# Kernel optimization log

Measured on AMD Instinct MI355X. Metric: run time of the kernel, lower is better.

Reference implementation:

```python
import jax, jax.numpy as jnp
import numpy as np

BN_EPS = 1e-5

def _ste_sign(x):
    # forward: sign in {-1,+1}; backward: clipped straight-through (grad 1 on [-1,1])
    s = jnp.where(x >= 0, 1.0, -1.0).astype(x.dtype)
    c = jnp.clip(x, -1.0, 1.0)
    return c + jax.lax.stop_gradient(s - c)

def setup_inputs() -> dict:
    key = jax.random.key(0)
    ks = jax.random.split(key, 8)
    N, C, H, W = 32, 256, 56, 56
    x = jax.random.normal(ks[0], (N, C, H, W), dtype=jnp.float32)
    bias0 = jax.random.normal(ks[1], (C,), dtype=jnp.float32) * 0.1
    w = jax.random.normal(ks[2], (C, C, 1, 1), dtype=jnp.float32) * 0.05
    gamma = jnp.ones((C,), dtype=jnp.float32)
    beta = jnp.zeros((C,), dtype=jnp.float32)
    bias1 = jax.random.normal(ks[3], (C,), dtype=jnp.float32) * 0.1
    alpha = jnp.full((C,), 0.25, dtype=jnp.float32)  # PReLU init
    bias2 = jax.random.normal(ks[4], (C,), dtype=jnp.float32) * 0.1
    return {"x": x, "bias0": bias0, "w": w, "gamma": gamma, "beta": beta,
            "bias1": bias1, "alpha": alpha, "bias2": bias2}

def reference(x, bias0, w, gamma, beta, bias1, alpha, bias2):
    ch = lambda v: v[None, :, None, None]
    # move0: learnable per-channel bias
    out = x + ch(bias0)
    # binary activation: sign (STE)
    out = _ste_sign(out)
    # binarized 1x1 conv: w_bin = mean(|w|) per out-channel * sign(w)
    scale = jnp.mean(jnp.abs(w), axis=(1, 2, 3))              # [O]
    wb = scale[:, None] * _ste_sign(w[:, :, 0, 0])            # [O, C]
    out = jnp.einsum('nchw,oc->nohw', out, wb)                # 1x1 conv
    # bn1: batch statistics (training-mode math)
    mu = jnp.mean(out, axis=(0, 2, 3), keepdims=True)
    var = jnp.var(out, axis=(0, 2, 3), keepdims=True)
    out = ch(gamma) * (out - mu) * jax.lax.rsqrt(var + BN_EPS) + ch(beta)
    # residual add (downsample is None)
    out = out + x
    # move1 -> PReLU -> move2
    out = out + ch(bias1)
    out = jnp.where(out > 0, out, ch(alpha) * out)
    out = out + ch(bias2)
    return out
```

## Files before the change

kernel.cpp:

```cpp
#include <hip/hip_runtime.h>
#include <stdint.h>

typedef unsigned long long u64;
typedef unsigned int u32;

constexpr int kC  = 256;
constexpr int kHW = 3136;
constexpr int kN  = 32;
constexpr int kP  = kN * kHW;
constexpr int kPB = 64;
constexpr int kBlocks = kP / kPB;

constexpr size_t OFF_T     = 0;
constexpr size_t OFF_SCALE = 8192;
constexpr size_t OFF_SUMD  = 9216;
constexpr size_t OFF_SUMD2 = 11264;
constexpr size_t OFF_S     = 13312;

__global__ __launch_bounds__(256) void prep_kernel(
    const float* __restrict__ w, char* __restrict__ ws) {
  u64*   T     = (u64*)(ws + OFF_T);
  float* scale = (float*)(ws + OFF_SCALE);
  u64*   sumd  = (u64*)(ws + OFF_SUMD);
  u64*   sumd2 = (u64*)(ws + OFF_SUMD2);

  int o = threadIdx.x;
  const float* wr = w + o * kC;
  float acc = 0.0f;
  u64 bits[4] = {0, 0, 0, 0};
#pragma unroll 8
  for (int c = 0; c < kC; ++c) {
    float v = wr[c];
    acc += fabsf(v);
    if (v >= 0.0f) bits[c >> 6] |= (1ull << (c & 63));
  }
  scale[o] = acc * (1.0f / 256.0f);
#pragma unroll
  for (int k = 0; k < 4; ++k) T[k * 256 + o] = bits[k];
  sumd[o]  = 0ull;
  sumd2[o] = 0ull;
}

__global__ __launch_bounds__(256) void pack_stats_kernel(
    const float* __restrict__ x, const float* __restrict__ bias0,
    char* __restrict__ ws) {
  __shared__ u64 ldsS[4][kPB];

  int t     = threadIdx.x;
  int pos   = t & 63;
  int chunk = t >> 6;

  u32 p  = blockIdx.x * (u32)kPB + (u32)pos;
  u32 n  = p / kHW;
  u32 hw = p - n * kHW;
  const float* xp = x + (size_t)n * kC * kHW + (size_t)(chunk * 64) * kHW + hw;
  const float* bp = bias0 + chunk * 64;

  u64 bits = 0;
#pragma unroll 16
  for (int i = 0; i < 64; ++i) {
    float v = xp[(size_t)i * kHW] + bp[i];
    if (v >= 0.0f) bits |= (1ull << i);
  }

  u64* S = (u64*)(ws + OFF_S);
  S[(size_t)chunk * kP + p] = bits;
  ldsS[chunk][pos] = bits;
  __syncthreads();

  const u64* T = (const u64*)(ws + OFF_T);
  u64 t0 = T[t], t1 = T[256 + t], t2 = T[512 + t], t3 = T[768 + t];
  int summ = 0, summ2 = 0;
#pragma unroll 8
  for (int pp = 0; pp < kPB; ++pp) {
    int k = __popcll(ldsS[0][pp] ^ t0) + __popcll(ldsS[1][pp] ^ t1) +
            __popcll(ldsS[2][pp] ^ t2) + __popcll(ldsS[3][pp] ^ t3);
    int m = 128 - k;
    summ  += m;
    summ2 += m * m;
  }
  u64* sumd  = (u64*)(ws + OFF_SUMD);
  u64* sumd2 = (u64*)(ws + OFF_SUMD2);
  atomicAdd(&sumd[t],  (u64)(long long)(2 * summ));
  atomicAdd(&sumd2[t], (u64)(long long)(4 * summ2));
}

__global__ __launch_bounds__(256) void finalize_kernel(
    const float* __restrict__ x, const float* __restrict__ gamma,
    const float* __restrict__ beta, const float* __restrict__ bias1,
    const float* __restrict__ alpha, const float* __restrict__ bias2,
    const char* __restrict__ ws, float* __restrict__ out) {
  __shared__ u64    ldsT[4][256];
  __shared__ float4 ldsC[256];

  int t = threadIdx.x;
  {
    const u64* T = (const u64*)(ws + OFF_T);
#pragma unroll
    for (int k = 0; k < 4; ++k) ldsT[k][t] = T[k * 256 + t];

    const float*     scale = (const float*)(ws + OFF_SCALE);
    const long long* sumd  = (const long long*)(ws + OFF_SUMD);
    const long long* sumd2 = (const long long*)(ws + OFF_SUMD2);
    double inv  = 1.0 / (double)kP;
    double md   = (double)sumd[t] * inv;
    double e2   = (double)sumd2[t] * inv;
    double vard = e2 - md * md;
    float sc  = scale[t];
    float mu  = sc * (float)md;
    float var = sc * sc * (float)vard;
    float rs  = rsqrtf(var + 1e-5f);
    float g   = gamma[t];
    float cA  = g * rs * sc;
    float cB  = beta[t] - g * rs * mu + bias1[t];
    ldsC[t] = make_float4(2.0f * cA, cB, alpha[t], bias2[t]);
  }
  __syncthreads();

  int pos   = t & 63;
  int chunk = t >> 6;
  u32 p  = blockIdx.x * (u32)kPB + (u32)pos;
  u32 n  = p / kHW;
  u32 hw = p - n * kHW;

  const u64* S = (const u64*)(ws + OFF_S);
  u64 s0 = S[p], s1 = S[kP + p], s2 = S[2 * kP + p], s3 = S[3 * kP + p];

  const float* xp = x   + (size_t)n * kC * kHW + (size_t)(chunk * 64) * kHW + hw;
  float*       op = out + (size_t)n * kC * kHW + (size_t)(chunk * 64) * kHW + hw;

#pragma unroll 8
  for (int i = 0; i < 64; ++i) {
    int o = chunk * 64 + i;
    int k = __popcll(s0 ^ ldsT[0][o]) + __popcll(s1 ^ ldsT[1][o]) +
            __popcll(s2 ^ ldsT[2][o]) + __popcll(s3 ^ ldsT[3][o]);
    float m  = (float)(128 - k);
    float4 cc = ldsC[o];
    float xv = xp[(size_t)i * kHW];
    float u  = fmaf(cc.x, m, cc.y) + xv;
    float r  = u > 0.0f ? u : cc.z * u;
    op[(size_t)i * kHW] = r + cc.w;
  }
}

extern "C" void kernel_launch(void* const* d_in, const int* in_sizes, int n_in,
                              void* d_out, int out_size, void* d_ws, size_t ws_size,
                              hipStream_t stream) {
  const float* x     = (const float*)d_in[0];
  const float* bias0 = (const float*)d_in[1];
  const float* w     = (const float*)d_in[2];
  const float* gamma = (const float*)d_in[3];
  const float* beta  = (const float*)d_in[4];
  const float* bias1 = (const float*)d_in[5];
  const float* alpha = (const float*)d_in[6];
  const float* bias2 = (const float*)d_in[7];
  float* out = (float*)d_out;
  char*  ws  = (char*)d_ws;

  hipLaunchKernelGGL(prep_kernel, dim3(1), dim3(256), 0, stream, w, ws);
  hipLaunchKernelGGL(pack_stats_kernel, dim3(kBlocks), dim3(256), 0, stream,
                     x, bias0, ws);
  hipLaunchKernelGGL(finalize_kernel, dim3(kBlocks), dim3(256), 0, stream,
                     x, gamma, beta, bias1, alpha, bias2, ws, out);
}
```

Measured before the change: 278.1 us.

## Split pack and stats kernels, process two positions per lane, parallelize weight prep

Weight preparation is spread across 16 blocks using wave ballots and shuffle reductions instead of a single serial thread loop. Packing now handles two adjacent pixels per lane with float2 loads and 16-byte stores, and the popcount-based batch statistics move into a separate kernel that reads the packed sign bits back from global memory. The finalize kernel likewise processes two positions per lane with vector loads and stores, and uses an output-major LDS layout for the weight bits. Together these aim to widen memory accesses and cut per-position overhead, at the cost of an extra launch and an extra global pass over the packed bits.

```diff
diff --git a/kernel.cpp b/kernel.cpp
--- a/kernel.cpp
+++ b/kernel.cpp
@@ -8,14 +8,16 @@
 constexpr int kHW = 3136;
 constexpr int kN  = 32;
 constexpr int kP  = kN * kHW;
-constexpr int kPB = 64;
-constexpr int kBlocks = kP / kPB;
+constexpr int kPosB = 128;
+constexpr int kBlocksP = kP / kPosB;
 
 constexpr size_t OFF_T     = 0;
 constexpr size_t OFF_SCALE = 8192;
 constexpr size_t OFF_SUMD  = 9216;
 constexpr size_t OFF_SUMD2 = 11264;
 constexpr size_t OFF_S     = 13312;
+
+struct alignas(16) U64x2 { u64 x, y; };
 
 __global__ __launch_bounds__(256) void prep_kernel(
     const float* __restrict__ w, char* __restrict__ ws) {
@@ -24,65 +26,80 @@
   u64*   sumd  = (u64*)(ws + OFF_SUMD);
   u64*   sumd2 = (u64*)(ws + OFF_SUMD2);
 
-  int o = threadIdx.x;
-  const float* wr = w + o * kC;
-  float acc = 0.0f;
-  u64 bits[4] = {0, 0, 0, 0};
-#pragma unroll 8
-  for (int c = 0; c < kC; ++c) {
-    float v = wr[c];
-    acc += fabsf(v);
-    if (v >= 0.0f) bits[c >> 6] |= (1ull << (c & 63));
+  int t = threadIdx.x;
+  int k = t >> 6, lane = t & 63;
+  int b = blockIdx.x;
+  if (b == 0) { sumd[t] = 0ull; sumd2[t] = 0ull; }
+
+  __shared__ float part[4][16];
+#pragma unroll
+  for (int i = 0; i < 16; ++i) {
+    int o = b * 16 + i;
+    float v = w[o * kC + k * 64 + lane];
+    u64 m = __ballot(v >= 0.0f);
+    float a = fabsf(v);
+#pragma unroll
+    for (int s = 32; s > 0; s >>= 1) a += __shfl_xor(a, s, 64);
+    if (lane == 0) { T[k * 256 + o] = m; part[k][i] = a; }
   }
-  scale[o] = acc * (1.0f / 256.0f);
-#pragma unroll
-  for (int k = 0; k < 4; ++k) T[k * 256 + o] = bits[k];
-  sumd[o]  = 0ull;
-  sumd2[o] = 0ull;
+  __syncthreads();
+  if (t < 16) {
+    int o = b * 16 + t;
+    scale[o] = (part[0][t] + part[1][t] + part[2][t] + part[3][t]) * (1.0f / 256.0f);
+  }
 }
 
-__global__ __launch_bounds__(256) void pack_stats_kernel(
+__global__ __launch_bounds__(256) void pack_kernel(
     const float* __restrict__ x, const float* __restrict__ bias0,
     char* __restrict__ ws) {
-  __shared__ u64 ldsS[4][kPB];
+  int t = threadIdx.x;
+  int k = __builtin_amdgcn_readfirstlane(t >> 6);
+  int lane = t & 63;
 
-  int t     = threadIdx.x;
-  int pos   = t & 63;
-  int chunk = t >> 6;
-
-  u32 p  = blockIdx.x * (u32)kPB + (u32)pos;
+  u32 p  = blockIdx.x * (u32)kPosB + 2u * lane;
   u32 n  = p / kHW;
   u32 hw = p - n * kHW;
-  const float* xp = x + (size_t)n * kC * kHW + (size_t)(chunk * 64) * kHW + hw;
-  const float* bp = bias0 + chunk * 64;
+  const float* xp = x + (size_t)n * kC * kHW + (size_t)(k * 64) * kHW + hw;
+  const float* bp = bias0 + k * 64;
 
-  u64 bits = 0;
+  u64 m0 = 0, m1 = 0;
 #pragma unroll 16
   for (int i = 0; i < 64; ++i) {
-    float v = xp[(size_t)i * kHW] + bp[i];
-    if (v >= 0.0f) bits |= (1ull << i);
+    float2 v = *(const float2*)(xp + (size_t)i * kHW);
+    float bb = bp[i];
+    m0 |= (u64)(v.x + bb >= 0.0f) << i;
+    m1 |= (u64)(v.y + bb >= 0.0f) << i;
   }
+  u64* S = (u64*)(ws + OFF_S);
+  U64x2 st; st.x = m0; st.y = m1;
+  *(U64x2*)&S[(size_t)k * kP + p] = st;
+}
 
-  u64* S = (u64*)(ws + OFF_S);
-  S[(size_t)chunk * kP + p] = bits;
-  ldsS[chunk][pos] = bits;
-  __syncthreads();
+__global__ __launch_bounds__(256) void stats_kernel(char* __restrict__ ws) {
+  int o = threadIdx.x;
+  const u64* T = (const u64*)(ws + OFF_T);
+  u64 t0 = T[o], t1 = T[256 + o], t2 = T[512 + o], t3 = T[768 + o];
+  const u64* S = (const u64*)(ws + OFF_S);
+  u32 pb = blockIdx.x * (u32)kPosB;
 
-  const u64* T = (const u64*)(ws + OFF_T);
-  u64 t0 = T[t], t1 = T[256 + t], t2 = T[512 + t], t3 = T[768 + t];
   int summ = 0, summ2 = 0;
 #pragma unroll 8
-  for (int pp = 0; pp < kPB; ++pp) {
-    int k = __popcll(ldsS[0][pp] ^ t0) + __popcll(ldsS[1][pp] ^ t1) +
-            __popcll(ldsS[2][pp] ^ t2) + __popcll(ldsS[3][pp] ^ t3);
-    int m = 128 - k;
-    summ  += m;
-    summ2 += m * m;
+  for (int j = 0; j < kPosB; j += 2) {
+    u32 p = pb + j;
+    U64x2 a0 = *(const U64x2*)&S[p];
+    U64x2 a1 = *(const U64x2*)&S[kP + p];
+    U64x2 a2 = *(const U64x2*)&S[2 * kP + p];
+    U64x2 a3 = *(const U64x2*)&S[3 * kP + p];
+    int ka = __popcll(a0.x ^ t0) + __popcll(a1.x ^ t1) +
+             __popcll(a2.x ^ t2) + __popcll(a3.x ^ t3);
+    int kb = __popcll(a0.y ^ t0) + __popcll(a1.y ^ t1) +
+             __popcll(a2.y ^ t2) + __popcll(a3.y ^ t3);
+    int ma = 128 - ka, mb = 128 - kb;
+    summ  += ma + mb;
+    summ2 += ma * ma + mb * mb;
   }
-  u64* sumd  = (u64*)(ws + OFF_SUMD);
-  u64* sumd2 = (u64*)(ws + OFF_SUMD2);
-  atomicAdd(&sumd[t],  (u64)(long long)(2 * summ));
-  atomicAdd(&sumd2[t], (u64)(long long)(4 * summ2));
+  atomicAdd((u64*)(ws + OFF_SUMD) + o,  (u64)(long long)(2 * summ));
+  atomicAdd((u64*)(ws + OFF_SUMD2) + o, (u64)(long long)(4 * summ2));
 }
 
 __global__ __launch_bounds__(256) void finalize_kernel(
@@ -90,14 +107,14 @@
     const float* __restrict__ beta, const float* __restrict__ bias1,
     const float* __restrict__ alpha, const float* __restrict__ bias2,
     const char* __restrict__ ws, float* __restrict__ out) {
-  __shared__ u64    ldsT[4][256];
+  __shared__ u64    ldsT[256][4];
   __shared__ float4 ldsC[256];
 
   int t = threadIdx.x;
   {
     const u64* T = (const u64*)(ws + OFF_T);
 #pragma unroll
-    for (int k = 0; k < 4; ++k) ldsT[k][t] = T[k * 256 + t];
+    for (int q = 0; q < 4; ++q) ldsT[t][q] = T[q * 256 + t];
 
     const float*     scale = (const float*)(ws + OFF_SCALE);
     const long long* sumd  = (const long long*)(ws + OFF_SUMD);
@@ -117,29 +134,37 @@
   }
   __syncthreads();
 
-  int pos   = t & 63;
-  int chunk = t >> 6;
-  u32 p  = blockIdx.x * (u32)kPB + (u32)pos;
+  int k = __builtin_amdgcn_readfirstlane(t >> 6);
+  int lane = t & 63;
+  u32 p  = blockIdx.x * (u32)kPosB + 2u * lane;
   u32 n  = p / kHW;
   u32 hw = p - n * kHW;
 
   const u64* S = (const u64*)(ws + OFF_S);
-  u64 s0 = S[p], s1 = S[kP + p], s2 = S[2 * kP + p], s3 = S[3 * kP + p];
+  U64x2 s0 = *(const U64x2*)&S[p];
+  U64x2 s1 = *(const U64x2*)&S[kP + p];
+  U64x2 s2 = *(const U64x2*)&S[2 * kP + p];
+  U64x2 s3 = *(const U64x2*)&S[3 * kP + p];
 
-  const float* xp = x   + (size_t)n * kC * kHW + (size_t)(chunk * 64) * kHW + hw;
-  float*       op = out + (size_t)n * kC * kHW + (size_t)(chunk * 64) * kHW + hw;
+  const float* xp = x   + (size_t)n * kC * kHW + (size_t)(k * 64) * kHW + hw;
+  float*       op = out + (size_t)n * kC * kHW + (size_t)(k * 64) * kHW + hw;
 
 #pragma unroll 8
   for (int i = 0; i < 64; ++i) {
-    int o = chunk * 64 + i;
-    int k = __popcll(s0 ^ ldsT[0][o]) + __popcll(s1 ^ ldsT[1][o]) +
-            __popcll(s2 ^ ldsT[2][o]) + __popcll(s3 ^ ldsT[3][o]);
-    float m  = (float)(128 - k);
+    int o = k * 64 + i;
+    u64 w0 = ldsT[o][0], w1 = ldsT[o][1], w2 = ldsT[o][2], w3 = ldsT[o][3];
+    int ka = __popcll(s0.x ^ w0) + __popcll(s1.x ^ w1) +
+             __popcll(s2.x ^ w2) + __popcll(s3.x ^ w3);
+    int kb = __popcll(s0.y ^ w0) + __popcll(s1.y ^ w1) +
+             __popcll(s2.y ^ w2) + __popcll(s3.y ^ w3);
     float4 cc = ldsC[o];
-    float xv = xp[(size_t)i * kHW];
-    float u  = fmaf(cc.x, m, cc.y) + xv;
-    float r  = u > 0.0f ? u : cc.z * u;
-    op[(size_t)i * kHW] = r + cc.w;
+    float2 xv = *(const float2*)(xp + (size_t)i * kHW);
+    float u0 = fmaf(cc.x, (float)(128 - ka), cc.y) + xv.x;
+    float u1 = fmaf(cc.x, (float)(128 - kb), cc.y) + xv.y;
+    float r0 = u0 > 0.0f ? u0 : cc.z * u0;
+    float r1 = u1 > 0.0f ? u1 : cc.z * u1;
+    float2 ov; ov.x = r0 + cc.w; ov.y = r1 + cc.w;
+    *(float2*)(op + (size_t)i * kHW) = ov;
   }
 }
 
@@ -157,9 +182,10 @@
   float* out = (float*)d_out;
   char*  ws  = (char*)d_ws;
 
-  hipLaunchKernelGGL(prep_kernel, dim3(1), dim3(256), 0, stream, w, ws);
-  hipLaunchKernelGGL(pack_stats_kernel, dim3(kBlocks), dim3(256), 0, stream,
+  hipLaunchKernelGGL(prep_kernel, dim3(16), dim3(256), 0, stream, w, ws);
+  hipLaunchKernelGGL(pack_kernel, dim3(kBlocksP), dim3(256), 0, stream,
                      x, bias0, ws);
-  hipLaunchKernelGGL(finalize_kernel, dim3(kBlocks), dim3(256), 0, stream,
+  hipLaunchKernelGGL(stats_kernel, dim3(kBlocksP), dim3(256), 0, stream, ws);
+  hipLaunchKernelGGL(finalize_kernel, dim3(kBlocksP), dim3(256), 0, stream,
                      x, gamma, beta, bias1, alpha, bias2, ws, out);
 }
```

Result: faster. 257.6 us (-7.4%).
